# Performance work log

Measured on AMD Instinct MI355X. Metric: run time of the kernel, lower is better.

The kernel has to match this reference:

```python
import jax, jax.numpy as jnp
import numpy as np

N = 200000      # active voxels
CIN = 64
COUT = 128
L = 96
EPS = 1e-5

# 27 kernel offsets for a 3x3x3 sparse conv (Minkowski region: [-1,0,1]^3)
_OFFS = np.array([[dx, dy, dz] for dx in (-1, 0, 1) for dy in (-1, 0, 1) for dz in (-1, 0, 1)], dtype=np.int64)


def _build_nbr_map():
    """Build [27, N] map: nbr_idx[k, i] = row of input voxel at coord_i + off_k, or N if absent."""
    rng = np.random.default_rng(0)
    keys = rng.choice(L ** 3, size=N, replace=False)           # unique voxel hashes
    coords = np.stack(np.unravel_index(keys, (L, L, L)), axis=1).astype(np.int64)  # [N,3]
    order = np.argsort(keys)
    skeys = keys[order]
    maps = np.full((27, N), N, dtype=np.int32)
    for k in range(27):
        q = coords + _OFFS[k]
        inb = np.all((q >= 0) & (q < L), axis=1)
        qk = (q[:, 0] * L + q[:, 1]) * L + q[:, 2]
        pos = np.searchsorted(skeys, qk)
        pos = np.clip(pos, 0, N - 1)
        hit = inb & (skeys[pos] == qk)
        maps[k] = np.where(hit, order[pos].astype(np.int32), N)
    return jnp.asarray(maps)


def setup_inputs() -> dict:
    key = jax.random.key(0)
    ks = jax.random.split(key, 4)
    feats = jax.random.normal(ks[0], (N, CIN), dtype=jnp.float32)
    W1 = jax.random.normal(ks[1], (27, CIN, COUT), dtype=jnp.float32) * (1.0 / np.sqrt(27 * CIN))
    W2 = jax.random.normal(ks[2], (27, COUT, COUT), dtype=jnp.float32) * (1.0 / np.sqrt(27 * COUT))
    Wsk = jax.random.normal(ks[3], (CIN, COUT), dtype=jnp.float32) * (1.0 / np.sqrt(CIN))
    ones = jnp.ones((COUT,), jnp.float32)
    zeros = jnp.zeros((COUT,), jnp.float32)
    return {
        "feats": feats, "nbr_idx": _build_nbr_map(),
        "W1": W1, "g1": ones, "b1": zeros,
        "W2": W2, "g2": ones, "b2": zeros,
        "Wsk": Wsk, "gsk": ones, "bsk": zeros,
    }


def _sparse_conv3(feats, nbr_idx, W):
    """Stride-1 3x3x3 sparse conv: out[i] = sum_k feats[nbr(i,k)] @ W[k]."""
    fpad = jnp.concatenate([feats, jnp.zeros((1, feats.shape[1]), feats.dtype)], axis=0)  # sentinel row N -> 0
    out = jnp.zeros((feats.shape[0], W.shape[2]), feats.dtype)
    for k in range(W.shape[0]):  # fixed 27 kernel taps
        out = out + fpad[nbr_idx[k]] @ W[k]
    return out


def _bn(x, g, b):
    m = jnp.mean(x, axis=0)
    v = jnp.var(x, axis=0)
    return (x - m) * jax.lax.rsqrt(v + EPS) * g + b


def reference(feats, nbr_idx, W1, g1, b1, W2, g2, b2, Wsk, gsk, bsk):
    # skip branch: 1x1 sparse conv (pointwise matmul) + BN
    skip = _bn(feats @ Wsk, gsk, bsk)
    # res branch: conv3 -> BN -> conv3 -> BN
    h = _bn(_sparse_conv3(feats, nbr_idx, W1), g1, b1)
    res = _bn(_sparse_conv3(h, nbr_idx, W2), g2, b2)
    return jax.nn.relu(res + skip)
```

## Files before the change

### kernel.cpp

```cpp
#include <hip/hip_runtime.h>
#include <stdint.h>

#define NV 200000
#define BN_EPS 1e-5f

typedef short bf16x8 __attribute__((ext_vector_type(8)));
typedef float f32x4 __attribute__((ext_vector_type(4)));

__device__ inline unsigned short f2bf(float x) {
  union { float f; uint32_t u; } c; c.f = x;
  uint32_t r = c.u + 0x7fffu + ((c.u >> 16) & 1u);
  return (unsigned short)(r >> 16);
}
__device__ inline float bf2f(unsigned short u) {
  union { uint32_t u; float f; } c; c.u = ((uint32_t)u) << 16;
  return c.f;
}

__device__ inline void gload_lds16(const void* g, void* l) {
  __builtin_amdgcn_global_load_lds(
      (const __attribute__((address_space(1))) unsigned int*)(g),
      (__attribute__((address_space(3))) unsigned int*)(l), 16, 0, 0);
}


#define STAGEW(v, buf)                                                       \
  do {                                                                       \
    const char* wsrc_ = (const char*)Wpack + (size_t)(v)*TAPBYTES;           \
    _Pragma("unroll") for (int i_ = 0; i_ < TAPBYTES / 4096; ++i_) {         \
      const int off_ = w * (TAPBYTES / 4) + i_ * 1024;                       \
      gload_lds16(wsrc_ + off_ + l * 16, (char*)(&Wlds[buf][0]) + off_);     \
    }                                                                        \
  } while (0)

#define LOADIDX(rt, d)                                                       \
  do {                                                                       \
    _Pragma("unroll") for (int rf_ = 0; rf_ < 4; ++rf_) {                    \
      const int row_ = rowbase + rf_ * 16 + l15;                             \
      int r_ = NV;                                                           \
      if (row_ < NV) r_ = GATHER ? nbr[(size_t)(rt)*NV + row_] : row_;       \
      d[rf_] = r_;                                                           \
    }                                                                        \
  } while (0)

#define GATHERS(ar, idx, voff)                                               \
  do {                                                                       \
    _Pragma("unroll") for (int rf_ = 0; rf_ < 4; ++rf_) {                    \
      const unsigned short* ap_ =                                            \
          Apad + (size_t)idx[rf_] * K + (voff) + lhi * 8;                    \
      _Pragma("unroll") for (int s_ = 0; s_ < 2; ++s_) ar[rf_][s_] =         \
          *(const bf16x8*)(ap_ + s_ * 32);                                   \
    }                                                                        \
  } while (0)

#define COMPUTE(ar, buf)                                                     \
  do {                                                                       \
    __builtin_amdgcn_s_setprio(1);                                           \
    _Pragma("unroll") for (int s_ = 0; s_ < 2; ++s_) {                       \
      bf16x8 b_[8];                                                          \
      _Pragma("unroll") for (int cf_ = 0; cf_ < 8; ++cf_) b_[cf_] =          \
          *(const bf16x8*)&Wlds[buf][((s_ * 8 + cf_) * 64 + l) * 8];         \
      _Pragma("unroll") for (int rf_ = 0; rf_ < 4; ++rf_)                    \
          _Pragma("unroll") for (int cf_ = 0; cf_ < 8; ++cf_) acc[rf_][cf_] =\
          __builtin_amdgcn_mfma_f32_16x16x32_bf16(ar[rf_][s_], b_[cf_],      \
                                                  acc[rf_][cf_], 0, 0, 0);   \
    }                                                                        \
    __builtin_amdgcn_s_setprio(0);                                           \
  } while (0)

template <int NTAPS, int KSPLIT, bool GATHER, bool OUTBF>
__global__ __launch_bounds__(256, 2) void conv_mfma(
    const unsigned short* __restrict__ Apad, const int* __restrict__ nbr,
    const unsigned short* __restrict__ Wpack, void* __restrict__ outp,
    float* __restrict__ ssum, float* __restrict__ ssq) {
  constexpr int KV = 64;
  constexpr int K = KV * KSPLIT;
  constexpr int TAPH = 2 * 8 * 64 * 8;
  constexpr int TAPBYTES = TAPH * 2;
  __shared__ unsigned short Wlds[2][TAPH];
  __shared__ float sred[4][128];

  const int tid = threadIdx.x;
  const int w = tid >> 6;
  const int l = tid & 63;
  const int l15 = l & 15;
  const int lhi = l >> 4;
  const int rowbase = blockIdx.x * 256 + w * 64;

  f32x4 acc[4][8];
#pragma unroll
  for (int rf = 0; rf < 4; ++rf)
#pragma unroll
    for (int cf = 0; cf < 8; ++cf) acc[rf][cf] = f32x4{0.f, 0.f, 0.f, 0.f};

  bf16x8 aregA[4][2], aregB[4][2];
  int idxA[4], idxB[4];

  if constexpr (KSPLIT == 1) {
    LOADIDX(0, idxA);
    STAGEW(0, 0);
    GATHERS(aregA, idxA, 0);
    if (NTAPS > 1) LOADIDX(1, idxB);
    __syncthreads();
    for (int t = 0; t < NTAPS; t += 2) {
      if (t + 1 < NTAPS) {
        STAGEW(t + 1, 1);
        GATHERS(aregB, idxB, 0);
        if (t + 2 < NTAPS) LOADIDX(t + 2, idxA);
      }
      COMPUTE(aregA, 0);
      __syncthreads();
      if (t + 1 < NTAPS) {
        if (t + 2 < NTAPS) {
          STAGEW(t + 2, 0);
          GATHERS(aregA, idxA, 0);
          if (t + 3 < NTAPS) LOADIDX(t + 3, idxB);
        }
        COMPUTE(aregB, 1);
        __syncthreads();
      }
    }
  } else {
    LOADIDX(0, idxA);
    STAGEW(0, 0);
    GATHERS(aregA, idxA, 0);
    __syncthreads();
    for (int rt = 0; rt < NTAPS; ++rt) {
      STAGEW(2 * rt + 1, 1);
      GATHERS(aregB, idxA, KV);
      if (rt + 1 < NTAPS) LOADIDX(rt + 1, idxB);
      COMPUTE(aregA, 0);
      __syncthreads();
      if (rt + 1 < NTAPS) {
        STAGEW(2 * rt + 2, 0);
        GATHERS(aregA, idxB, 0);
#pragma unroll
        for (int rf = 0; rf < 4; ++rf) idxA[rf] = idxB[rf];
      }
      COMPUTE(aregB, 1);
      __syncthreads();
    }
  }

  float psum[8], psq[8];
#pragma unroll
  for (int cf = 0; cf < 8; ++cf) {
    float s = 0.f, q = 0.f;
#pragma unroll
    for (int rf = 0; rf < 4; ++rf)
#pragma unroll
      for (int v = 0; v < 4; ++v) {
        const float x = acc[rf][cf][v];
        s += x;
        q += x * x;
      }
    psum[cf] = s;
    psq[cf] = q;
  }
#pragma unroll
  for (int cf = 0; cf < 8; ++cf) {
    psum[cf] += __shfl_xor(psum[cf], 16);
    psum[cf] += __shfl_xor(psum[cf], 32);
    psq[cf] += __shfl_xor(psq[cf], 16);
    psq[cf] += __shfl_xor(psq[cf], 32);
  }
  if (l < 16) {
#pragma unroll
    for (int cf = 0; cf < 8; ++cf) sred[w][cf * 16 + l] = psum[cf];
  }
  __syncthreads();
  if (tid < 128)
    atomicAdd(&ssum[tid], sred[0][tid] + sred[1][tid] + sred[2][tid] + sred[3][tid]);
  __syncthreads();
  if (l < 16) {
#pragma unroll
    for (int cf = 0; cf < 8; ++cf) sred[w][cf * 16 + l] = psq[cf];
  }
  __syncthreads();
  if (tid < 128)
    atomicAdd(&ssq[tid], sred[0][tid] + sred[1][tid] + sred[2][tid] + sred[3][tid]);

#pragma unroll
  for (int rf = 0; rf < 4; ++rf) {
#pragma unroll
    for (int v = 0; v < 4; ++v) {
      const int row = rowbase + rf * 16 + lhi * 4 + v;
      if (row < NV) {
#pragma unroll
        for (int cf = 0; cf < 8; ++cf) {
          const float x = acc[rf][cf][v];
          if (OUTBF)
            ((unsigned short*)outp)[(size_t)row * 128 + cf * 16 + l15] = f2bf(x);
          else
            ((float*)outp)[(size_t)row * 128 + cf * 16 + l15] = x;
        }
      }
    }
  }
}

__global__ void pack_w_kernel(const float* __restrict__ W,
                              unsigned short* __restrict__ o, int sshift,
                              int total) {
  const int e = blockIdx.x * blockDim.x + threadIdx.x;
  if (e >= total) return;
  const int j = e & 7;
  const int l = (e >> 3) & 63;
  const int cf = (e >> 9) & 7;
  const int ts = e >> 12;
  const int S = 1 << sshift;
  const int s = ts & (S - 1);
  const int tap = ts >> sshift;
  const int kk = s * 32 + (l >> 4) * 8 + j;
  const int col = cf * 16 + (l & 15);
  o[e] = f2bf(W[((size_t)tap * (S * 32) + kk) * 128 + col]);
}

__global__ void feats_to_bf16(const float* __restrict__ f,
                              unsigned short* __restrict__ o) {
  const int i = blockIdx.x * blockDim.x + threadIdx.x;
  if (i >= (NV + 1) * 16) return;
  const int row = i >> 4;
  const int c = (i & 15) * 4;
  ushort4 ov;
  if (row < NV) {
    const float4 v = *(const float4*)(f + (size_t)row * 64 + c);
    ov.x = f2bf(v.x);
    ov.y = f2bf(v.y);
    ov.z = f2bf(v.z);
    ov.w = f2bf(v.w);
  } else {
    ov = make_ushort4(0, 0, 0, 0);
  }
  *(ushort4*)(o + (size_t)row * 64 + c) = ov;
}

__global__ void zero_stats(float* st) {
  const int t = blockIdx.x * 256 + threadIdx.x;
  if (t < 768) st[t] = 0.f;
}

__global__ void finalize1(float* st, const float* g1, const float* b1,
                          const float* gsk, const float* bsk) {
  const float invN = 1.0f / NV;
  const int t = threadIdx.x;
  if (t < 128) {
    const float m = st[t] * invN;
    const float v = st[128 + t] * invN - m * m;
    const float sc = g1[t] * rsqrtf(v + BN_EPS);
    st[768 + t] = sc;
    st[896 + t] = b1[t] - m * sc;
  } else {
    const int c = t - 128;
    const float m = st[256 + c] * invN;
    const float v = st[384 + c] * invN - m * m;
    const float sc = gsk[c] * rsqrtf(v + BN_EPS);
    st[1024 + c] = sc;
    st[1152 + c] = bsk[c] - m * sc;
  }
}

__global__ void finalize2(float* st, const float* g2, const float* b2) {
  const float invN = 1.0f / NV;
  const int c = threadIdx.x;
  const float m = st[512 + c] * invN;
  const float v = st[640 + c] * invN - m * m;
  const float sc = g2[c] * rsqrtf(v + BN_EPS);
  st[1280 + c] = sc;
  st[1408 + c] = b2[c] - m * sc;
}

__global__ void bn_to_bf16(const unsigned short* __restrict__ raw,
                           const float* __restrict__ scale,
                           const float* __restrict__ bias,
                           unsigned short* __restrict__ outp) {
  const int i = blockIdx.x * blockDim.x + threadIdx.x;
  if (i >= (NV + 1) * 32) return;
  const int row = i >> 5;
  const int c = (i & 31) * 4;
  ushort4 ov;
  if (row < NV) {
    const ushort4 rv = *(const ushort4*)(raw + (size_t)row * 128 + c);
    ov.x = f2bf(bf2f(rv.x) * scale[c + 0] + bias[c + 0]);
    ov.y = f2bf(bf2f(rv.y) * scale[c + 1] + bias[c + 1]);
    ov.z = f2bf(bf2f(rv.z) * scale[c + 2] + bias[c + 2]);
    ov.w = f2bf(bf2f(rv.w) * scale[c + 3] + bias[c + 3]);
  } else {
    ov = make_ushort4(0, 0, 0, 0);
  }
  *(ushort4*)(outp + (size_t)row * 128 + c) = ov;
}

__global__ void final_kernel(float* __restrict__ outp,
                             const unsigned short* __restrict__ c2,
                             const unsigned short* __restrict__ sk,
                             const float* __restrict__ st) {
  const int i = blockIdx.x * blockDim.x + threadIdx.x;
  if (i >= NV * 32) return;
  const int row = i >> 5;
  const int c = (i & 31) * 4;
  const float* s2 = st + 1280;
  const float* b2 = st + 1408;
  const float* ss = st + 1024;
  const float* bs = st + 1152;
  const ushort4 rv = *(const ushort4*)(c2 + (size_t)row * 128 + c);
  const ushort4 kv = *(const ushort4*)(sk + (size_t)row * 128 + c);
  float4 o;
  o.x = fmaxf(0.f, bf2f(rv.x) * s2[c + 0] + b2[c + 0] + bf2f(kv.x) * ss[c + 0] + bs[c + 0]);
  o.y = fmaxf(0.f, bf2f(rv.y) * s2[c + 1] + b2[c + 1] + bf2f(kv.y) * ss[c + 1] + bs[c + 1]);
  o.z = fmaxf(0.f, bf2f(rv.z) * s2[c + 2] + b2[c + 2] + bf2f(kv.z) * ss[c + 2] + bs[c + 2]);
  o.w = fmaxf(0.f, bf2f(rv.w) * s2[c + 3] + b2[c + 3] + bf2f(kv.w) * ss[c + 3] + bs[c + 3]);
  *(float4*)(outp + (size_t)row * 128 + c) = o;
}

extern "C" void kernel_launch(void* const* d_in, const int* in_sizes, int n_in,
                              void* d_out, int out_size, void* d_ws,
                              size_t ws_size, hipStream_t stream) {
  const float* feats = (const float*)d_in[0];
  const int* nbr = (const int*)d_in[1];
  const float* W1 = (const float*)d_in[2];
  const float* g1 = (const float*)d_in[3];
  const float* b1 = (const float*)d_in[4];
  const float* W2 = (const float*)d_in[5];
  const float* g2 = (const float*)d_in[6];
  const float* b2 = (const float*)d_in[7];
  const float* Wsk = (const float*)d_in[8];
  const float* gsk = (const float*)d_in[9];
  const float* bsk = (const float*)d_in[10];

  char* ws = (char*)d_ws;
  auto align = [](size_t x) { return (x + 255) & ~(size_t)255; };
  size_t off = 0;
  float* stats = (float*)(ws + off);
  off = align(off + 12 * 128 * 4);
  unsigned short* w1p = (unsigned short*)(ws + off);
  off = align(off + (size_t)27 * 2 * 8 * 64 * 8 * 2);
  unsigned short* w2p = (unsigned short*)(ws + off);
  off = align(off + (size_t)27 * 4 * 8 * 64 * 8 * 2);
  unsigned short* wskp = (unsigned short*)(ws + off);
  off = align(off + (size_t)2 * 8 * 64 * 8 * 2);
  unsigned short* fbf = (unsigned short*)(ws + off);
  off = align(off + (size_t)(NV + 1) * 64 * 2);
  unsigned short* c1 = (unsigned short*)(ws + off);
  off = align(off + (size_t)NV * 128 * 2);
  unsigned short* skr = (unsigned short*)(ws + off);
  off = align(off + (size_t)NV * 128 * 2);
  unsigned short* hbf = (unsigned short*)(ws + off);
  off = align(off + (size_t)(NV + 1) * 128 * 2);

  float* out = (float*)d_out;

  zero_stats<<<3, 256, 0, stream>>>(stats);
  const int t1 = 27 * 2 * 8 * 64 * 8;
  pack_w_kernel<<<(t1 + 255) / 256, 256, 0, stream>>>(W1, w1p, 1, t1);
  const int t2 = 27 * 4 * 8 * 64 * 8;
  pack_w_kernel<<<(t2 + 255) / 256, 256, 0, stream>>>(W2, w2p, 2, t2);
  const int t3 = 2 * 8 * 64 * 8;
  pack_w_kernel<<<(t3 + 255) / 256, 256, 0, stream>>>(Wsk, wskp, 1, t3);
  feats_to_bf16<<<((NV + 1) * 16 + 255) / 256, 256, 0, stream>>>(feats, fbf);

  const int convBlocks = (NV + 255) / 256;
  conv_mfma<27, 1, true, true>
      <<<convBlocks, 256, 0, stream>>>(fbf, nbr, w1p, c1, stats + 0, stats + 128);
  conv_mfma<1, 1, false, true>
      <<<convBlocks, 256, 0, stream>>>(fbf, nullptr, wskp, skr, stats + 256, stats + 384);
  finalize1<<<1, 256, 0, stream>>>(stats, g1, b1, gsk, bsk);
  bn_to_bf16<<<((NV + 1) * 32 + 255) / 256, 256, 0, stream>>>(c1, stats + 768,
                                                              stats + 896, hbf);
  conv_mfma<27, 2, true, true>
      <<<convBlocks, 256, 0, stream>>>(hbf, nbr, w2p, c1, stats + 512, stats + 640);
  finalize2<<<1, 128, 0, stream>>>(stats, g2, b2);
  final_kernel<<<(NV * 32 + 255) / 256, 256, 0, stream>>>(out, c1, skr, stats);
}
```

Before: 522.4 us.

## Halve conv block size to two waves and precompute 32-bit gather byte offsets

The conv kernels now launch 128-thread blocks (two waves, 128 rows) instead of 256 threads. Each block still stages the full per-tap weight slice into LDS, with each wave copying half. Neighbour indices are turned into 32-bit byte offsets once when loaded, which removes the 64-bit multiply-add address math from each gather. Smaller blocks mean more blocks and fewer waves sharing each LDS weight tile, so weight staging traffic per row doubles and block-level stats atomics also double.

Measured after the change: 675.2 us. 1.29x slower.

```diff
diff --git a/kernel.cpp b/kernel.cpp
--- a/kernel.cpp
+++ b/kernel.cpp
@@ -27,29 +27,28 @@
 #define STAGEW(v, buf)                                                       \
   do {                                                                       \
     const char* wsrc_ = (const char*)Wpack + (size_t)(v)*TAPBYTES;           \
-    _Pragma("unroll") for (int i_ = 0; i_ < TAPBYTES / 4096; ++i_) {         \
-      const int off_ = w * (TAPBYTES / 4) + i_ * 1024;                       \
+    _Pragma("unroll") for (int i_ = 0; i_ < 8; ++i_) {                       \
+      const int off_ = w * 8192 + i_ * 1024;                                 \
       gload_lds16(wsrc_ + off_ + l * 16, (char*)(&Wlds[buf][0]) + off_);     \
     }                                                                        \
   } while (0)
 
-#define LOADIDX(rt, d)                                                       \
+#define LOADOFF(rt, d)                                                       \
   do {                                                                       \
     _Pragma("unroll") for (int rf_ = 0; rf_ < 4; ++rf_) {                    \
       const int row_ = rowbase + rf_ * 16 + l15;                             \
       int r_ = NV;                                                           \
       if (row_ < NV) r_ = GATHER ? nbr[(size_t)(rt)*NV + row_] : row_;       \
-      d[rf_] = r_;                                                           \
+      d[rf_] = ((uint32_t)r_ << SH) + lhi * 16;                              \
     }                                                                        \
   } while (0)
 
-#define GATHERS(ar, idx, voff)                                               \
+#define GATHERS(ar, vo, vb)                                                  \
   do {                                                                       \
     _Pragma("unroll") for (int rf_ = 0; rf_ < 4; ++rf_) {                    \
-      const unsigned short* ap_ =                                            \
-          Apad + (size_t)idx[rf_] * K + (voff) + lhi * 8;                    \
+      const char* ap_ = (const char*)Apad + (size_t)vo[rf_];                 \
       _Pragma("unroll") for (int s_ = 0; s_ < 2; ++s_) ar[rf_][s_] =         \
-          *(const bf16x8*)(ap_ + s_ * 32);                                   \
+          *(const bf16x8*)(ap_ + (vb) + s_ * 64);                            \
     }                                                                        \
   } while (0)
 
@@ -69,23 +68,22 @@
   } while (0)
 
 template <int NTAPS, int KSPLIT, bool GATHER, bool OUTBF>
-__global__ __launch_bounds__(256, 2) void conv_mfma(
+__global__ __launch_bounds__(128, 2) void conv_mfma(
     const unsigned short* __restrict__ Apad, const int* __restrict__ nbr,
     const unsigned short* __restrict__ Wpack, void* __restrict__ outp,
     float* __restrict__ ssum, float* __restrict__ ssq) {
-  constexpr int KV = 64;
-  constexpr int K = KV * KSPLIT;
+  constexpr int SH = (KSPLIT == 2) ? 8 : 7;
   constexpr int TAPH = 2 * 8 * 64 * 8;
   constexpr int TAPBYTES = TAPH * 2;
   __shared__ unsigned short Wlds[2][TAPH];
-  __shared__ float sred[4][128];
+  __shared__ float sred[2][128];
 
   const int tid = threadIdx.x;
   const int w = tid >> 6;
   const int l = tid & 63;
   const int l15 = l & 15;
   const int lhi = l >> 4;
-  const int rowbase = blockIdx.x * 256 + w * 64;
+  const int rowbase = blockIdx.x * 128 + w * 64;
 
   f32x4 acc[4][8];
 #pragma unroll
@@ -94,48 +92,48 @@
     for (int cf = 0; cf < 8; ++cf) acc[rf][cf] = f32x4{0.f, 0.f, 0.f, 0.f};
 
   bf16x8 aregA[4][2], aregB[4][2];
-  int idxA[4], idxB[4];
+  uint32_t offA[4], offB[4];
 
   if constexpr (KSPLIT == 1) {
-    LOADIDX(0, idxA);
+    LOADOFF(0, offA);
     STAGEW(0, 0);
-    GATHERS(aregA, idxA, 0);
-    if (NTAPS > 1) LOADIDX(1, idxB);
+    GATHERS(aregA, offA, 0);
+    if (NTAPS > 1) LOADOFF(1, offB);
     __syncthreads();
     for (int t = 0; t < NTAPS; t += 2) {
       if (t + 1 < NTAPS) {
         STAGEW(t + 1, 1);
-        GATHERS(aregB, idxB, 0);
-        if (t + 2 < NTAPS) LOADIDX(t + 2, idxA);
+        GATHERS(aregB, offB, 0);
+        if (t + 2 < NTAPS) LOADOFF(t + 2, offA);
       }
       COMPUTE(aregA, 0);
       __syncthreads();
       if (t + 1 < NTAPS) {
         if (t + 2 < NTAPS) {
           STAGEW(t + 2, 0);
-          GATHERS(aregA, idxA, 0);
-          if (t + 3 < NTAPS) LOADIDX(t + 3, idxB);
+          GATHERS(aregA, offA, 0);
+          if (t + 3 < NTAPS) LOADOFF(t + 3, offB);
         }
         COMPUTE(aregB, 1);
         __syncthreads();
       }
     }
   } else {
-    LOADIDX(0, idxA);
+    LOADOFF(0, offA);
     STAGEW(0, 0);
-    GATHERS(aregA, idxA, 0);
+    GATHERS(aregA, offA, 0);
     __syncthreads();
     for (int rt = 0; rt < NTAPS; ++rt) {
       STAGEW(2 * rt + 1, 1);
-      GATHERS(aregB, idxA, KV);
-      if (rt + 1 < NTAPS) LOADIDX(rt + 1, idxB);
+      GATHERS(aregB, offA, 128);
+      if (rt + 1 < NTAPS) LOADOFF(rt + 1, offB);
       COMPUTE(aregA, 0);
       __syncthreads();
       if (rt + 1 < NTAPS) {
         STAGEW(2 * rt + 2, 0);
-        GATHERS(aregA, idxB, 0);
-#pragma unroll
-        for (int rf = 0; rf < 4; ++rf) idxA[rf] = idxB[rf];
+        GATHERS(aregA, offB, 0);
+#pragma unroll
+        for (int rf = 0; rf < 4; ++rf) offA[rf] = offB[rf];
       }
       COMPUTE(aregB, 1);
       __syncthreads();
@@ -169,16 +167,14 @@
     for (int cf = 0; cf < 8; ++cf) sred[w][cf * 16 + l] = psum[cf];
   }
   __syncthreads();
-  if (tid < 128)
-    atomicAdd(&ssum[tid], sred[0][tid] + sred[1][tid] + sred[2][tid] + sred[3][tid]);
+  atomicAdd(&ssum[tid], sred[0][tid] + sred[1][tid]);
   __syncthreads();
   if (l < 16) {
 #pragma unroll
     for (int cf = 0; cf < 8; ++cf) sred[w][cf * 16 + l] = psq[cf];
   }
   __syncthreads();
-  if (tid < 128)
-    atomicAdd(&ssq[tid], sred[0][tid] + sred[1][tid] + sred[2][tid] + sred[3][tid]);
+  atomicAdd(&ssq[tid], sred[0][tid] + sred[1][tid]);
 
 #pragma unroll
   for (int rf = 0; rf < 4; ++rf) {
@@ -359,16 +355,16 @@
   pack_w_kernel<<<(t3 + 255) / 256, 256, 0, stream>>>(Wsk, wskp, 1, t3);
   feats_to_bf16<<<((NV + 1) * 16 + 255) / 256, 256, 0, stream>>>(feats, fbf);
 
-  const int convBlocks = (NV + 255) / 256;
+  const int convBlocks = (NV + 127) / 128;
   conv_mfma<27, 1, true, true>
-      <<<convBlocks, 256, 0, stream>>>(fbf, nbr, w1p, c1, stats + 0, stats + 128);
+      <<<convBlocks, 128, 0, stream>>>(fbf, nbr, w1p, c1, stats + 0, stats + 128);
   conv_mfma<1, 1, false, true>
-      <<<convBlocks, 256, 0, stream>>>(fbf, nullptr, wskp, skr, stats + 256, stats + 384);
+      <<<convBlocks, 128, 0, stream>>>(fbf, nullptr, wskp, skr, stats + 256, stats + 384);
   finalize1<<<1, 256, 0, stream>>>(stats, g1, b1, gsk, bsk);
   bn_to_bf16<<<((NV + 1) * 32 + 255) / 256, 256, 0, stream>>>(c1, stats + 768,
                                                               stats + 896, hbf);
   conv_mfma<27, 2, true, true>
-      <<<convBlocks, 256, 0, stream>>>(hbf, nbr, w2p, c1, stats + 512, stats + 640);
+      <<<convBlocks, 128, 0, stream>>>(hbf, nbr, w2p, c1, stats + 512, stats + 640);
   finalize2<<<1, 128, 0, stream>>>(stats, g2, b2);
   final_kernel<<<(NV * 32 + 255) / 256, 256, 0, stream>>>(out, c1, skr, stats);
 }
```
